# Performance work log

Hardware: AMD Instinct MI355X
Metric: run time of the kernel (lower is better)

The kernel has to match this reference:

```python
import jax, jax.numpy as jnp
import numpy as np

B, N, IN_FEAT, HID, NHEAD, NLAYER, K = 8, 2048, 512, 128, 4, 3, 8
GRAPH_DIM = 32
EPS = 1e-5


def _layernorm(x, g, b):
    m = x.mean(-1, keepdims=True)
    v = ((x - m) ** 2).mean(-1, keepdims=True)
    return (x - m) * jax.lax.rsqrt(v + EPS) * g + b


def _knn_adj(cent):
    # cent [B,Ni,2] -> symmetric bool adjacency [B,Ni,Ni]; each node's k nearest
    # neighbours (self included, dist 0), then bidirected union (to_bidirected).
    d2 = jnp.sum((cent[:, :, None, :] - cent[:, None, :, :]) ** 2, -1)
    _, idx = jax.lax.top_k(-d2, K)  # [B,Ni,K]
    Bc, Nc = cent.shape[0], cent.shape[1]
    mask = jnp.zeros((Bc, Nc, Nc), bool).at[
        jnp.arange(Bc)[:, None, None], jnp.arange(Nc)[None, :, None], idx].set(True)
    return mask | jnp.swapaxes(mask, 1, 2)


def setup_inputs():
    key = jax.random.key(0)
    ks = jax.random.split(key, 12)
    s = 0.05
    H = HID
    return dict(
        feats=jax.random.normal(ks[0], (B, N, IN_FEAT), jnp.float32),
        cent=jax.random.uniform(ks[1], (B, N, 2), jnp.float32),
        Wp1=jax.random.normal(ks[2], (IN_FEAT, H)) * s, bp1=jnp.zeros((H,)),
        bn_g=jnp.ones((H,)), bn_b=jnp.zeros((H,)),
        Wp2=jax.random.normal(ks[3], (H, H)) * s, bp2=jnp.zeros((H,)),
        g1=jnp.ones((NLAYER, H)), be1=jnp.zeros((NLAYER, H)),
        g2=jnp.ones((NLAYER, H)), be2=jnp.zeros((NLAYER, H)),
        Ws=jax.random.normal(ks[4], (NLAYER, NHEAD, H, H)) * s,
        Wn=jax.random.normal(ks[5], (NLAYER, NHEAD, H, H)) * s,
        bs=jnp.zeros((NLAYER, NHEAD, H)),
        Wg=jax.random.normal(ks[6], (NLAYER, NHEAD * H, H)) * s,
        bg=jnp.zeros((NLAYER, H)),
        W1=jax.random.normal(ks[7], (NLAYER, H, H)) * s, b1=jnp.zeros((NLAYER, H)),
        W2=jax.random.normal(ks[8], (NLAYER, H, H)) * s, b2=jnp.zeros((NLAYER, H)),
        Wq=jax.random.normal(ks[9], (NLAYER, H, 1)) * s, bq=jnp.zeros((NLAYER,)),
        Wf1=jax.random.normal(ks[10], (2 * H, H)) * s, bf1=jnp.zeros((H,)),
        Wf2=jax.random.normal(ks[11], (H, GRAPH_DIM)) * s, bf2=jnp.zeros((GRAPH_DIM,)),
    )


def reference(feats, cent, Wp1, bp1, bn_g, bn_b, Wp2, bp2,
              g1, be1, g2, be2, Ws, Wn, bs, Wg, bg,
              W1, b1, W2, b2, Wq, bq, Wf1, bf1, Wf2, bf2):
    # preconv: Linear -> BatchNorm1d(eval: running mean 0 / var 1) -> ReLU -> Linear
    x = feats @ Wp1 + bp1
    x = x * (bn_g / jnp.sqrt(1.0 + EPS)) + bn_b
    x = jax.nn.relu(x) @ Wp2 + bp2              # [B,N,H]
    c = cent
    picks = 0.0
    for i in range(NLAYER):
        A = _knn_adj(c).astype(x.dtype)          # dynamic KNN graph, [B,Ni,Ni]
        deg = A.sum(-1)                          # in-degree (>=1, self loop)
        # GraphTransformerLayer: pre-LN -> multi-head mean SAGEConv -> residual
        xn = _layernorm(x, g1[i], be1[i])
        m = jnp.einsum('bij,bjd->bid', A, xn) / deg[..., None]
        h = jnp.einsum('bnd,hde->bnhe', xn, Ws[i]) \
            + jnp.einsum('bnd,hde->bnhe', m, Wn[i]) + bs[i]
        Bc, Nc = h.shape[0], h.shape[1]
        h = h.reshape(Bc, Nc, NHEAD * HID)       # concat heads on feature dim
        x = x + jax.nn.relu(h) @ Wg[i] + bg[i]
        # FFN block with residual
        xn2 = _layernorm(x, g2[i], be2[i])
        x = x + jax.nn.relu(xn2 @ W1[i] + b1[i]) @ W2[i] + b2[i]
        # SAGPool: GraphConv (symmetric norm) score -> top-k ratio 0.5 -> gate
        dinv = jax.lax.rsqrt(deg)
        s = dinv * jnp.einsum('bij,bj->bi', A, dinv * (x @ Wq[i])[..., 0]) + bq[i]
        kkeep = Nc // 2
        topv, topi = jax.lax.top_k(s, kkeep)     # per-graph top nodes
        x = jnp.take_along_axis(x, topi[..., None], axis=1) * jnp.tanh(topv)[..., None]
        c = jnp.take_along_axis(c, topi[..., None], axis=1)
        # max + avg readout on pooled graph
        picks = picks + jnp.concatenate([x.max(axis=1), x.mean(axis=1)], axis=-1)
    f = jax.nn.relu(picks @ Wf1 + bf1)
    f = jax.nn.relu(f @ Wf2 + bf2)               # [B, GRAPH_DIM]
    return f
```

## Files before the change

### kernel.cpp

```cpp
#include <hip/hip_runtime.h>
#include <math.h>

#define EPSV 1e-5f
#define GF_RELU 1
#define GF_ACCUM 2

typedef unsigned long long u64;
typedef unsigned int u32;
typedef unsigned short u16;
typedef float v2f __attribute__((ext_vector_type(2)));
typedef short bf16x8 __attribute__((ext_vector_type(8)));
typedef float f32x4 __attribute__((ext_vector_type(4)));

static const int Bn = 8;
static const int Nmax = 2048;
static const int KNN_K = 8;

__device__ __forceinline__ u32 split_pack(float v) {
  u32 u = __float_as_uint(v);
  float r = v - __uint_as_float(u & 0xffff0000u);
  return (u >> 16) | (__float_as_uint(r) & 0xffff0000u);
}

__device__ __forceinline__ void split4(float4 v, uint2& hp, uint2& lp) {
  u32 u0 = __float_as_uint(v.x), u1 = __float_as_uint(v.y);
  u32 u2 = __float_as_uint(v.z), u3 = __float_as_uint(v.w);
  float r0 = v.x - __uint_as_float(u0 & 0xffff0000u);
  float r1 = v.y - __uint_as_float(u1 & 0xffff0000u);
  float r2 = v.z - __uint_as_float(u2 & 0xffff0000u);
  float r3 = v.w - __uint_as_float(u3 & 0xffff0000u);
  hp.x = (u0 >> 16) | (u1 & 0xffff0000u);
  hp.y = (u2 >> 16) | (u3 & 0xffff0000u);
  lp.x = (__float_as_uint(r0) >> 16) | (__float_as_uint(r1) & 0xffff0000u);
  lp.y = (__float_as_uint(r2) >> 16) | (__float_as_uint(r3) & 0xffff0000u);
}

__device__ __forceinline__ void depair4(uint4 p, uint2& hp, uint2& lp) {
  hp.x = (p.x & 0xffffu) | (p.y << 16);
  hp.y = (p.z & 0xffffu) | (p.w << 16);
  lp.x = (p.x >> 16) | (p.y & 0xffff0000u);
  lp.y = (p.z >> 16) | (p.w & 0xffff0000u);
}

__global__ void precompute_kernel(const float* __restrict__ bn_g, const float* __restrict__ bn_b,
                                  const float* __restrict__ bp1,
                                  float* __restrict__ sc, float* __restrict__ bb,
                                  float* __restrict__ picks) {
  int t = threadIdx.x;
  if (t < 128) {
    float s = bn_g[t] / sqrtf(1.0f + EPSV);
    sc[t] = s;
    bb[t] = bp1[t] * s + bn_b[t];
  }
  for (int i = t; i < Bn * 256; i += blockDim.x) picks[i] = 0.0f;
}

__global__ void repack_ws_kernel(const float* __restrict__ Ws, const float* __restrict__ Wn,
                                 float* __restrict__ WsP, float* __restrict__ WnP) {
  int idx = blockIdx.x * 256 + threadIdx.x;
  const int total = 3 * 4 * 128 * 128;
  if (idx >= total) return;
  int e = idx & 127, d = (idx >> 7) & 127, h = (idx >> 14) & 3, L = idx >> 16;
  size_t dst = ((size_t)L * 128 + d) * 512 + h * 128 + e;
  WsP[dst] = Ws[idx];
  WnP[dst] = Wn[idx];
}

__global__ void repack_split_kernel(const float* __restrict__ Ws, const float* __restrict__ Wn,
                                    const float* __restrict__ Wg, const float* __restrict__ Wp1,
                                    const float* __restrict__ Wp2, const float* __restrict__ W1,
                                    const float* __restrict__ W2,
                                    u32* __restrict__ Wc,
                                    u16* __restrict__ WgTh, u16* __restrict__ WgTl,
                                    u32* __restrict__ Wp1T, u32* __restrict__ Wp2T,
                                    u16* __restrict__ W1Th, u16* __restrict__ W1Tl,
                                    u16* __restrict__ W2Th, u16* __restrict__ W2Tl) {
  int idx = blockIdx.x * 256 + threadIdx.x;
  if (idx < 393216) {
    int k = idx & 255, col = (idx >> 8) & 511, L = idx >> 17;
    float v;
    if (k < 128)
      v = Ws[(((size_t)(L * 4 + (col >> 7))) * 128 + k) * 128 + (col & 127)];
    else
      v = Wn[(((size_t)(L * 4 + (col >> 7))) * 128 + (k - 128)) * 128 + (col & 127)];
    Wc[idx] = split_pack(v);
  } else if (idx < 589824) {
    int i2 = idx - 393216;
    int k = i2 & 511, col = (i2 >> 9) & 127, L = i2 >> 16;
    u32 pr = split_pack(Wg[((size_t)L * 512 + k) * 128 + col]);
    size_t a = (size_t)L * 65536 + (size_t)(col >> 4) * 8192 +
               (size_t)(k >> 3) * 128 + (col & 15) * 8 + (k & 7);
    WgTh[a] = (u16)pr;
    WgTl[a] = (u16)(pr >> 16);
  } else if (idx < 655360) {
    int i3 = idx - 589824;
    int k = i3 & 511, col = i3 >> 9;
    Wp1T[i3] = split_pack(Wp1[(size_t)k * 128 + col]);
  } else if (idx < 671744) {
    int i4 = idx - 655360;
    int k = i4 & 127, col = i4 >> 7;
    Wp2T[i4] = split_pack(Wp2[(size_t)k * 128 + col]);
  } else if (idx < 720896) {
    int i5 = idx - 671744;
    int k = i5 & 127, col = (i5 >> 7) & 127, L = i5 >> 14;
    u32 pr = split_pack(W1[((size_t)L * 128 + k) * 128 + col]);
    size_t a = (size_t)L * 16384 + (size_t)(col >> 4) * 2048 +
               (size_t)(k >> 3) * 128 + (col & 15) * 8 + (k & 7);
    W1Th[a] = (u16)pr;
    W1Tl[a] = (u16)(pr >> 16);
  } else if (idx < 770048) {
    int i6 = idx - 720896;
    int k = i6 & 127, col = (i6 >> 7) & 127, L = i6 >> 14;
    u32 pr = split_pack(W2[((size_t)L * 128 + k) * 128 + col]);
    size_t a = (size_t)L * 16384 + (size_t)(col >> 4) * 2048 +
               (size_t)(k >> 3) * 128 + (col & 15) * 8 + (k & 7);
    W2Th[a] = (u16)pr;
    W2Tl[a] = (u16)(pr >> 16);
  }
}

template<int T>
__global__ __launch_bounds__(256) void knn_sel_kernel(const float* __restrict__ cent,
                                                      int* __restrict__ knn_idx, int Ni) {
  int i = blockIdx.x * 4 + (threadIdx.x >> 6);
  int b = blockIdx.y, lane = threadIdx.x & 63;
  const float2* cb = (const float2*)(cent + (size_t)b * Ni * 2);
  float2 ci = cb[i];
  u32 d2b[T];
#pragma unroll
  for (int t = 0; t < T; ++t) {
    int j = (t << 6) + lane;
    float2 cj = cb[j];
    float dx = __fsub_rn(ci.x, cj.x);
    float dy = __fsub_rn(ci.y, cj.y);
    float d2 = __fadd_rn(__fmul_rn(dx, dx), __fmul_rn(dy, dy));
    d2b[t] = __float_as_uint(d2);
  }
  constexpr int G = T / 4;
  u32 gmin[G];
  int gidx[G];
#pragma unroll
  for (int g = 0; g < G; ++g) {
    u32 m = d2b[g * 4]; int mi = g * 4;
#pragma unroll
    for (int e = 1; e < 4; ++e) {
      if (d2b[g * 4 + e] < m) { m = d2b[g * 4 + e]; mi = g * 4 + e; }
    }
    gmin[g] = m; gidx[g] = mi;
  }
  for (int r = 0; r < KNN_K; ++r) {
    u32 bd; int bt;
    if (G >= 2) {
      u32 a = gmin[0]; int ai = gidx[0];
      u32 bv = gmin[G / 2]; int bi = gidx[G / 2];
#pragma unroll
      for (int g = 1; g < G / 2; ++g) {
        if (gmin[g] < a) { a = gmin[g]; ai = gidx[g]; }
        if (gmin[G / 2 + g] < bv) { bv = gmin[G / 2 + g]; bi = gidx[G / 2 + g]; }
      }
      bd = a; bt = ai;
      if (bv < bd) { bd = bv; bt = bi; }
    } else {
      bd = gmin[0]; bt = gidx[0];
    }
    u64 key = ((u64)bd << 32) | (u32)((bt << 6) | lane);
    for (int off = 32; off >= 1; off >>= 1) {
      u64 o = __shfl_xor(key, off, 64);
      if (o < key) key = o;
    }
    u32 jsel = (u32)key;
    if (lane == 0) knn_idx[((size_t)(b * Ni + i)) * KNN_K + r] = (int)jsel;
    int tsel = __builtin_amdgcn_readfirstlane((int)(jsel >> 6));
    bool owner = (int)(jsel & 63) == lane;
    int gsel = tsel >> 2;
#pragma unroll
    for (int g = 0; g < G; ++g) {
      if (g == gsel) {
        if (owner) {
#pragma unroll
          for (int e = 0; e < 4; ++e)
            if (g * 4 + e == tsel) d2b[g * 4 + e] = 0xFFFFFFFFu;
          u32 m = d2b[g * 4]; int mi = g * 4;
#pragma unroll
          for (int e = 1; e < 4; ++e)
            if (d2b[g * 4 + e] < m) { m = d2b[g * 4 + e]; mi = g * 4 + e; }
          gmin[g] = m; gidx[g] = mi;
        }
      }
    }
  }
}

__global__ void build_adj_kernel(const int* __restrict__ knn_idx, u32* __restrict__ adj, int Ni) {
  int e = blockIdx.x * blockDim.x + threadIdx.x;
  int total = Bn * Ni * KNN_K;
  if (e >= total) return;
  int b = e / (Ni * KNN_K);
  int rem = e % (Ni * KNN_K);
  int r = rem / KNN_K;
  int j = knn_idx[e];
  atomicOr(&adj[((size_t)(b * Nmax + r)) * 64 + (j >> 5)], 1u << (j & 31));
  atomicOr(&adj[((size_t)(b * Nmax + j)) * 64 + (r >> 5)], 1u << (r & 31));
}

__global__ __launch_bounds__(256) void layernorm_kernel(const float* __restrict__ x,
                                                        const float* __restrict__ g,
                                                        const float* __restrict__ be,
                                                        float* __restrict__ xn) {
  int row = blockIdx.x * 4 + (threadIdx.x >> 6);
  int lane = threadIdx.x & 63;
  const float* xr = x + (size_t)row * 128;
  float v1 = xr[lane], v2 = xr[lane + 64];
  float s = v1 + v2;
  for (int off = 32; off >= 1; off >>= 1) s += __shfl_xor(s, off, 64);
  float mean = s / 128.0f;
  float d1 = v1 - mean, d2 = v2 - mean;
  float q = d1 * d1 + d2 * d2;
  for (int off = 32; off >= 1; off >>= 1) q += __shfl_xor(q, off, 64);
  float rs = rsqrtf(q / 128.0f + EPSV);
  float* xo = xn + (size_t)row * 128;
  xo[lane] = d1 * rs * g[lane] + be[lane];
  xo[lane + 64] = d2 * rs * g[lane + 64] + be[lane + 64];
}

__global__ __launch_bounds__(256) void aggregate_kernel(const u32* __restrict__ adj,
                                                        const float* __restrict__ xn,
                                                        float* __restrict__ m,
                                                        float* __restrict__ dinv, int Ni) {
  int sub = threadIdx.x >> 7;
  int t = threadIdx.x & 127;
  int i = blockIdx.x * 2 + sub, b = blockIdx.y;
  __shared__ int cnt[2];
  extern __shared__ int list[];
  int* lst = list + sub * Ni;
  if (t == 0) cnt[sub] = 0;
  __syncthreads();
  int wpr = Ni >> 5;
  for (int w = t; w < wpr; w += 128) {
    u32 bits = adj[((size_t)(b * Nmax + i)) * 64 + w];
    while (bits) {
      int bit = __ffs(bits) - 1;
      bits &= bits - 1;
      int pos = atomicAdd(&cnt[sub], 1);
      lst[pos] = (w << 5) + bit;
    }
  }
  __syncthreads();
  int d = cnt[sub];
  float a0 = 0.0f, a1 = 0.0f;
  int k = 0;
  for (; k + 2 <= d; k += 2) {
    a0 += xn[((size_t)b * Ni + lst[k]) * 128 + t];
    a1 += xn[((size_t)b * Ni + lst[k + 1]) * 128 + t];
  }
  if (k < d) a0 += xn[((size_t)b * Ni + lst[k]) * 128 + t];
  m[((size_t)b * Ni + i) * 128 + t] = (a0 + a1) / (float)d;
  if (t == 0) dinv[b * Nmax + i] = 1.0f / sqrtf((float)d);
}

__global__ __launch_bounds__(256) void attn_gemm1_kernel(
    const float* __restrict__ XN, const float* __restrict__ MM,
    const u32* __restrict__ Wc, const float* __restrict__ bs,
    u16* __restrict__ Hh, u16* __restrict__ Hl, int M) {
  __shared__ u16 Ah[128][40], Al[128][40], Bh[128][40], Bl[128][40];
  int tid = threadIdx.x;
  int lane = tid & 63, w = tid >> 6;
  int wr = w >> 1, wc = w & 1;
  int lr = lane & 15, lk = (lane >> 4) * 8;
  int rowBase = blockIdx.y * 128, colBase = blockIdx.x * 128;
  f32x4 acc[4][4] = {};
  int arow = tid >> 1, aq = (tid & 1) * 16;
  int bcol = tid >> 1, bq = (tid & 1) * 16;

  float4 af[4];
  uint4 bf[4];
  {
    const float* Ap = XN + (size_t)(rowBase + arow) * 128 + aq;
#pragma unroll
    for (int q = 0; q < 4; ++q) af[q] = *(const float4*)(Ap + 4 * q);
    const u32* Bp = Wc + (size_t)(colBase + bcol) * 256 + bq;
#pragma unroll
    for (int q = 0; q < 4; ++q) bf[q] = *(const uint4*)(Bp + 4 * q);
  }
  for (int t = 0; t < 8; ++t) {
    __syncthreads();
#pragma unroll
    for (int q = 0; q < 4; ++q) {
      uint2 hp, lp;
      split4(af[q], hp, lp);
      *(uint2*)&Ah[arow][aq + 4 * q] = hp;
      *(uint2*)&Al[arow][aq + 4 * q] = lp;
      depair4(bf[q], hp, lp);
      *(uint2*)&Bh[bcol][bq + 4 * q] = hp;
      *(uint2*)&Bl[bcol][bq + 4 * q] = lp;
    }
    __syncthreads();
    if (t + 1 < 8) {
      const float* Asrc = (t + 1 < 4) ? XN : MM;
      int k0 = ((t + 1) & 3) * 32;
      const float* Ap = Asrc + (size_t)(rowBase + arow) * 128 + k0 + aq;
#pragma unroll
      for (int q = 0; q < 4; ++q) af[q] = *(const float4*)(Ap + 4 * q);
      const u32* Bp = Wc + (size_t)(colBase + bcol) * 256 + (t + 1) * 32 + bq;
#pragma unroll
      for (int q = 0; q < 4; ++q) bf[q] = *(const uint4*)(Bp + 4 * q);
    }
    bf16x8 ah[4], al[4], bh[4], bl[4];
#pragma unroll
    for (int mi = 0; mi < 4; ++mi) {
      int ar = wr * 64 + mi * 16 + lr;
      ah[mi] = *(const bf16x8*)&Ah[ar][lk];
      al[mi] = *(const bf16x8*)&Al[ar][lk];
    }
#pragma unroll
    for (int ni = 0; ni < 4; ++ni) {
      int bc = wc * 64 + ni * 16 + lr;
      bh[ni] = *(const bf16x8*)&Bh[bc][lk];
      bl[ni] = *(const bf16x8*)&Bl[bc][lk];
    }
#pragma unroll
    for (int mi = 0; mi < 4; ++mi)
#pragma unroll
      for (int ni = 0; ni < 4; ++ni) {
        f32x4 c = acc[mi][ni];
        c = __builtin_amdgcn_mfma_f32_16x16x32_bf16(al[mi], bh[ni], c, 0, 0, 0);
        c = __builtin_amdgcn_mfma_f32_16x16x32_bf16(ah[mi], bl[ni], c, 0, 0, 0);
        c = __builtin_amdgcn_mfma_f32_16x16x32_bf16(ah[mi], bh[ni], c, 0, 0, 0);
        acc[mi][ni] = c;
      }
  }
  int rq = (lane >> 4) * 4;
#pragma unroll
  for (int ni = 0; ni < 4; ++ni) {
    int col = colBase + wc * 64 + ni * 16 + lr;
    float bv = bs[col];
    size_t cbase = (size_t)(col >> 3) * 128 + (col & 7);
#pragma unroll
    for (int mi = 0; mi < 4; ++mi) {
      int rb = (rowBase >> 4) + wr * 4 + mi;
#pragma unroll
      for (int r = 0; r < 4; ++r) {
        float v = fmaxf(acc[mi][ni][r] + bv, 0.0f);
        u32 pr = split_pack(v);
        size_t o = (size_t)rb * 8192 + cbase + (size_t)(rq + r) * 8;
        Hh[o] = (u16)pr;
        Hl[o] = (u16)(pr >> 16);
      }
    }
  }
}

__global__ __launch_bounds__(256) void attn2_ffn16_kernel(
    const u16* __restrict__ Hh, const u16* __restrict__ Hl,
    const u16* __restrict__ Bgh, const u16* __restrict__ Bgl,
    const float* __restrict__ bg, const float* __restrict__ g,
    const float* __restrict__ be,
    const u16* __restrict__ W1h, const u16* __restrict__ W1l,
    const float* __restrict__ b1,
    const u16* __restrict__ W2h, const u16* __restrict__ W2l,
    const float* __restrict__ b2, float* __restrict__ x,
    const float* __restrict__ Wq, const float* __restrict__ dinv,
    float* __restrict__ PV, int niShift, int M) {
  __shared__ float XF[16][132];
  __shared__ u16 XH[16][136], XL[16][136];
  __shared__ float QS[16];
  int tid = threadIdx.x;
  int lane = tid & 63, w = tid >> 6;
  int lr = lane & 15, lk = (lane >> 4) * 8, rq = (lane >> 4) * 4;
  int rowBase = blockIdx.x * 16;
  int colW = w * 32;
  int fo = (lane >> 4) * 128 + lr * 8;

  f32x4 acc[2] = {};
  {
    const u16* pAh = Hh + (size_t)blockIdx.x * 8192;
    const u16* pAl = Hl + (size_t)blockIdx.x * 8192;
    const u16* pBh = Bgh + (size_t)(w * 2) * 8192;
    const u16* pBl = Bgl + (size_t)(w * 2) * 8192;
    bf16x8 ah = *(const bf16x8*)(pAh + fo);
    bf16x8 al = *(const bf16x8*)(pAl + fo);
    bf16x8 b0h = *(const bf16x8*)(pBh + fo);
    bf16x8 b0l = *(const bf16x8*)(pBl + fo);
    bf16x8 b1h = *(const bf16x8*)(pBh + 8192 + fo);
    bf16x8 b1l = *(const bf16x8*)(pBl + 8192 + fo);
    for (int kt = 0; kt < 16; ++kt) {
      bf16x8 cah = ah, cal = al, cb0h = b0h, cb0l = b0l, cb1h = b1h, cb1l = b1l;
      if (kt + 1 < 16) {
        int off = (kt + 1) * 512 + fo;
        ah = *(const bf16x8*)(pAh + off);
        al = *(const bf16x8*)(pAl + off);
        b0h = *(const bf16x8*)(pBh + off);
        b0l = *(const bf16x8*)(pBl + off);
        b1h = *(const bf16x8*)(pBh + 8192 + off);
        b1l = *(const bf16x8*)(pBl + 8192 + off);
      }
      acc[0] = __builtin_amdgcn_mfma_f32_16x16x32_bf16(cal, cb0h, acc[0], 0, 0, 0);
      acc[0] = __builtin_amdgcn_mfma_f32_16x16x32_bf16(cah, cb0l, acc[0], 0, 0, 0);
      acc[0] = __builtin_amdgcn_mfma_f32_16x16x32_bf16(cah, cb0h, acc[0], 0, 0, 0);
      acc[1] = __builtin_amdgcn_mfma_f32_16x16x32_bf16(cal, cb1h, acc[1], 0, 0, 0);
      acc[1] = __builtin_amdgcn_mfma_f32_16x16x32_bf16(cah, cb1l, acc[1], 0, 0, 0);
      acc[1] = __builtin_amdgcn_mfma_f32_16x16x32_bf16(cah, cb1h, acc[1], 0, 0, 0);
    }
  }
#pragma unroll
  for (int ni = 0; ni < 2; ++ni) {
    int col = colW + ni * 16 + lr;
    float bv = bg[col];
#pragma unroll
    for (int r = 0; r < 4; ++r) {
      int rowL = rq + r;
      size_t o = (size_t)(rowBase + rowL) * 128 + col;
      float v = x[o] + acc[ni][r] + bv;
      x[o] = v;
      XF[rowL][col] = v;
    }
  }
  __syncthreads();
#pragma unroll
  for (int rr = 0; rr < 4; ++rr) {
    int rowL = w * 4 + rr;
    float v1 = XF[rowL][lane], v2 = XF[rowL][64 + lane];
    float s = v1 + v2;
    for (int off = 32; off >= 1; off >>= 1) s += __shfl_xor(s, off, 64);
    float mean = s / 128.0f;
    float d1 = v1 - mean, d2 = v2 - mean;
    float q = d1 * d1 + d2 * d2;
    for (int off = 32; off >= 1; off >>= 1) q += __shfl_xor(q, off, 64);
    float rs = rsqrtf(q / 128.0f + EPSV);
    float xn1 = d1 * rs * g[lane] + be[lane];
    float xn2 = d2 * rs * g[lane + 64] + be[lane + 64];
    u32 p1 = split_pack(xn1);
    u32 p2 = split_pack(xn2);
    XH[rowL][lane] = (u16)p1;  XL[rowL][lane] = (u16)(p1 >> 16);
    XH[rowL][64 + lane] = (u16)p2;  XL[rowL][64 + lane] = (u16)(p2 >> 16);
  }
  __syncthreads();
  f32x4 acc1[2] = {};
  {
    const u16* pBh = W1h + (size_t)(w * 2) * 2048;
    const u16* pBl = W1l + (size_t)(w * 2) * 2048;
#pragma unroll
    for (int kt = 0; kt < 4; ++kt) {
      int k0 = kt * 32 + lk;
      int off = kt * 512 + fo;
      bf16x8 ah = *(const bf16x8*)&XH[lr][k0];
      bf16x8 al = *(const bf16x8*)&XL[lr][k0];
      bf16x8 b0h = *(const bf16x8*)(pBh + off);
      bf16x8 b0l = *(const bf16x8*)(pBl + off);
      bf16x8 b1h = *(const bf16x8*)(pBh + 2048 + off);
      bf16x8 b1l = *(const bf16x8*)(pBl + 2048 + off);
      acc1[0] = __builtin_amdgcn_mfma_f32_16x16x32_bf16(al, b0h, acc1[0], 0, 0, 0);
      acc1[0] = __builtin_amdgcn_mfma_f32_16x16x32_bf16(ah, b0l, acc1[0], 0, 0, 0);
      acc1[0] = __builtin_amdgcn_mfma_f32_16x16x32_bf16(ah, b0h, acc1[0], 0, 0, 0);
      acc1[1] = __builtin_amdgcn_mfma_f32_16x16x32_bf16(al, b1h, acc1[1], 0, 0, 0);
      acc1[1] = __builtin_amdgcn_mfma_f32_16x16x32_bf16(ah, b1l, acc1[1], 0, 0, 0);
      acc1[1] = __builtin_amdgcn_mfma_f32_16x16x32_bf16(ah, b1h, acc1[1], 0, 0, 0);
    }
  }
  __syncthreads();
  if (tid < 16) QS[tid] = 0.0f;
#pragma unroll
  for (int ni = 0; ni < 2; ++ni) {
    int col = colW + ni * 16 + lr;
    float bv = b1[col];
#pragma unroll
    for (int r = 0; r < 4; ++r) {
      int rowL = rq + r;
      float v = fmaxf(acc1[ni][r] + bv, 0.0f);
      u32 pr = split_pack(v);
      XH[rowL][col] = (u16)pr;
      XL[rowL][col] = (u16)(pr >> 16);
    }
  }
  __syncthreads();
  f32x4 acc2[2] = {};
  {
    const u16* pBh = W2h + (size_t)(w * 2) * 2048;
    const u16* pBl = W2l + (size_t)(w * 2) * 2048;
#pragma unroll
    for (int kt = 0; kt < 4; ++kt) {
      int k0 = kt * 32 + lk;
      int off = kt * 512 + fo;
      bf16x8 ah = *(const bf16x8*)&XH[lr][k0];
      bf16x8 al = *(const bf16x8*)&XL[lr][k0];
      bf16x8 b0h = *(const bf16x8*)(pBh + off);
      bf16x8 b0l = *(const bf16x8*)(pBl + off);
      bf16x8 b1h = *(const bf16x8*)(pBh + 2048 + off);
      bf16x8 b1l = *(const bf16x8*)(pBl + 2048 + off);
      acc2[0] = __builtin_amdgcn_mfma_f32_16x16x32_bf16(al, b0h, acc2[0], 0, 0, 0);
      acc2[0] = __builtin_amdgcn_mfma_f32_16x16x32_bf16(ah, b0l, acc2[0], 0, 0, 0);
      acc2[0] = __builtin_amdgcn_mfma_f32_16x16x32_bf16(ah, b0h, acc2[0], 0, 0, 0);
      acc2[1] = __builtin_amdgcn_mfma_f32_16x16x32_bf16(al, b1h, acc2[1], 0, 0, 0);
      acc2[1] = __builtin_amdgcn_mfma_f32_16x16x32_bf16(ah, b1l, acc2[1], 0, 0, 0);
      acc2[1] = __builtin_amdgcn_mfma_f32_16x16x32_bf16(ah, b1h, acc2[1], 0, 0, 0);
    }
  }
  float qp[4] = {0.0f, 0.0f, 0.0f, 0.0f};
#pragma unroll
  for (int ni = 0; ni < 2; ++ni) {
    int col = colW + ni * 16 + lr;
    float bv = b2[col];
    float wq = Wq[col];
#pragma unroll
    for (int r = 0; r < 4; ++r) {
      int rowL = rq + r;
      size_t o = (size_t)(rowBase + rowL) * 128 + col;
      float v = x[o] + acc2[ni][r] + bv;
      x[o] = v;
      qp[r] += v * wq;
    }
  }
#pragma unroll
  for (int r = 0; r < 4; ++r) {
    qp[r] += __shfl_xor(qp[r], 1, 64);
    qp[r] += __shfl_xor(qp[r], 2, 64);
    qp[r] += __shfl_xor(qp[r], 4, 64);
    qp[r] += __shfl_xor(qp[r], 8, 64);
  }
  if (lr == 0) {
#pragma unroll
    for (int r = 0; r < 4; ++r) atomicAdd(&QS[rq + r], qp[r]);
  }
  __syncthreads();
  if (tid < 16) {
    int node = rowBase + tid;
    int bb = node >> niShift;
    int ii = node & ((1 << niShift) - 1);
    PV[bb * Nmax + ii] = dinv[bb * Nmax + ii] * QS[tid];
  }
}

__global__ __launch_bounds__(256) void preconv1_kernel(
    const float* __restrict__ F, const u32* __restrict__ WT,
    const float* __restrict__ sc, const float* __restrict__ bb,
    u32* __restrict__ H, int M) {
  __shared__ u16 Ah[64][40], Al[64][40], Bh[128][40], Bl[128][40];
  int tid = threadIdx.x;
  int lane = tid & 63, w = tid >> 6;
  int wr = w >> 1, wc = w & 1;
  int lr = lane & 15, lk = (lane >> 4) * 8;
  int rowBase = blockIdx.x * 64;
  f32x4 acc[2][4] = {};
  int arow = tid >> 2, aq = (tid & 3) * 8;
  int bcol = tid >> 1, bq = (tid & 1) * 16;

  float4 af[2];
  uint4 bf[4];
  {
    const float* Ap = F + (size_t)(rowBase + arow) * 512 + aq;
    af[0] = *(const float4*)Ap;
    af[1] = *(const float4*)(Ap + 4);
    const u32* Bp = WT + (size_t)bcol * 512 + bq;
#pragma unroll
    for (int q = 0; q < 4; ++q) bf[q] = *(const uint4*)(Bp + 4 * q);
  }
  for (int t = 0; t < 16; ++t) {
    __syncthreads();
    {
      uint2 hp, lp;
      split4(af[0], hp, lp);
      *(uint2*)&Ah[arow][aq] = hp; *(uint2*)&Al[arow][aq] = lp;
      split4(af[1], hp, lp);
      *(uint2*)&Ah[arow][aq + 4] = hp; *(uint2*)&Al[arow][aq + 4] = lp;
#pragma unroll
      for (int q = 0; q < 4; ++q) {
        depair4(bf[q], hp, lp);
        *(uint2*)&Bh[bcol][bq + 4 * q] = hp;
        *(uint2*)&Bl[bcol][bq + 4 * q] = lp;
      }
    }
    __syncthreads();
    if (t + 1 < 16) {
      int k0 = (t + 1) * 32;
      const float* Ap = F + (size_t)(rowBase + arow) * 512 + k0 + aq;
      af[0] = *(const float4*)Ap;
      af[1] = *(const float4*)(Ap + 4);
      const u32* Bp = WT + (size_t)bcol * 512 + k0 + bq;
#pragma unroll
      for (int q = 0; q < 4; ++q) bf[q] = *(const uint4*)(Bp + 4 * q);
    }
    bf16x8 ah[2], al[2], bh[4], bl[4];
#pragma unroll
    for (int mi = 0; mi < 2; ++mi) {
      int ar = wr * 32 + mi * 16 + lr;
      ah[mi] = *(const bf16x8*)&Ah[ar][lk];
      al[mi] = *(const bf16x8*)&Al[ar][lk];
    }
#pragma unroll
    for (int ni = 0; ni < 4; ++ni) {
      int bc = wc * 64 + ni * 16 + lr;
      bh[ni] = *(const bf16x8*)&Bh[bc][lk];
      bl[ni] = *(const bf16x8*)&Bl[bc][lk];
    }
#pragma unroll
    for (int mi = 0; mi < 2; ++mi)
#pragma unroll
      for (int ni = 0; ni < 4; ++ni) {
        f32x4 c = acc[mi][ni];
        c = __builtin_amdgcn_mfma_f32_16x16x32_bf16(al[mi], bh[ni], c, 0, 0, 0);
        c = __builtin_amdgcn_mfma_f32_16x16x32_bf16(ah[mi], bl[ni], c, 0, 0, 0);
        c = __builtin_amdgcn_mfma_f32_16x16x32_bf16(ah[mi], bh[ni], c, 0, 0, 0);
        acc[mi][ni] = c;
      }
  }
  int rq = (lane >> 4) * 4;
#pragma unroll
  for (int ni = 0; ni < 4; ++ni) {
    int col = wc * 64 + ni * 16 + lr;
    float s = sc[col], b = bb[col];
#pragma unroll
    for (int mi = 0; mi < 2; ++mi)
#pragma unroll
      for (int r = 0; r < 4; ++r) {
        int row = rowBase + wr * 32 + mi * 16 + rq + r;
        float v = fmaxf(acc[mi][ni][r] * s + b, 0.0f);
// ... 647 lines not shown
    }
  }
  v2f oacc[4][2] = {};
  {
    float4 q0 = *(const float4*)(W2 + (size_t)bk * 128 + bc);
    float4 q1 = *(const float4*)(W2 + (size_t)bk * 128 + bc + 4);
    for (int kt = 0; kt < 8; ++kt) {
      __syncthreads();
      *(float4*)&Bs[bk * 132 + bc] = q0;
      *(float4*)&Bs[bk * 132 + bc + 4] = q1;
      __syncthreads();
      if (kt < 7) {
        q0 = *(const float4*)(W2 + (size_t)(kt * 16 + 16 + bk) * 128 + bc);
        q1 = *(const float4*)(W2 + (size_t)(kt * 16 + 16 + bk) * 128 + bc + 4);
      }
      int k0 = kt * 16;
#pragma unroll
      for (int kk = 0; kk < 16; ++kk) {
        float av[4];
        v2f bv[2];
        *(float4*)av = *(const float4*)&Hs[(k0 + kk) * 36 + ty * 4];
        *(float4*)&bv[0] = *(const float4*)&Bs[kk * 132 + tx * 4];
#pragma unroll
        for (int r = 0; r < 4; ++r)
#pragma unroll
          for (int c = 0; c < 2; ++c) oacc[r][c] += av[r] * bv[c];
      }
    }
  }
#pragma unroll
  for (int r = 0; r < 4; ++r) {
    int row = rowBase + ty * 4 + r;
    float ov[4];
    *(v2f*)&ov[0] = oacc[r][0];
    *(v2f*)&ov[2] = oacc[r][1];
    float4 old = *(float4*)&x[(size_t)row * 128 + tx * 4];
    float4 v;
    v.x = ov[0] + b2[tx * 4 + 0]; v.x += old.x;
    v.y = ov[1] + b2[tx * 4 + 1]; v.y += old.y;
    v.z = ov[2] + b2[tx * 4 + 2]; v.z += old.z;
    v.w = ov[3] + b2[tx * 4 + 3]; v.w += old.w;
    *(float4*)&x[(size_t)row * 128 + tx * 4] = v;
  }
}

__global__ __launch_bounds__(256) void qp_kernel(const float* __restrict__ x,
                                                 const float* __restrict__ Wq,
                                                 const float* __restrict__ dinv,
                                                 float* __restrict__ p, int Ni) {
  int node = blockIdx.x * 4 + (threadIdx.x >> 6);
  int lane = threadIdx.x & 63;
  int b = node / Ni, i = node % Ni;
  float v = x[(size_t)node * 128 + lane] * Wq[lane] +
            x[(size_t)node * 128 + 64 + lane] * Wq[64 + lane];
  for (int off = 32; off >= 1; off >>= 1) v += __shfl_xor(v, off, 64);
  if (lane == 0) p[b * Nmax + i] = dinv[b * Nmax + i] * v;
}

__global__ __launch_bounds__(256) void score_kernel(const u32* __restrict__ adj,
                                                    const float* __restrict__ p,
                                                    const float* __restrict__ dinv,
                                                    const float* __restrict__ bq,
                                                    float* __restrict__ s, int Ni) {
  int i = blockIdx.x * 4 + (threadIdx.x >> 6);
  int b = blockIdx.y, lane = threadIdx.x & 63;
  int wpr = Ni >> 5;
  float acc = 0.0f;
  if (lane < wpr) {
    u32 bits = adj[((size_t)(b * Nmax + i)) * 64 + lane];
    while (bits) {
      int bit = __ffs(bits) - 1;
      bits &= bits - 1;
      acc += p[b * Nmax + (lane << 5) + bit];
    }
  }
  for (int off = 32; off >= 1; off >>= 1) acc += __shfl_xor(acc, off, 64);
  if (lane == 0) s[b * Nmax + i] = dinv[b * Nmax + i] * acc + bq[0];
}

__global__ void topk_rank_kernel(const float* __restrict__ s, int Ni, int* __restrict__ topi) {
  int b = blockIdx.y;
  int e0 = blockIdx.x * 64;
  int t = threadIdx.x;
  __shared__ u64 keys[2048];
  __shared__ int PR[256];
  for (int e = t; e < Ni; e += 256) {
    u32 u = __float_as_uint(s[b * Nmax + e]);
    u32 mono = (u & 0x80000000u) ? ~u : (u | 0x80000000u);
    keys[e] = ((u64)(~mono) << 32) | (u32)e;
  }
  __syncthreads();
  int quad = t >> 6, eloc = t & 63;
  u64 my = keys[e0 + eloc];
  int seg = Ni >> 2;
  int s0 = quad * seg;
  int rank = 0;
  for (int k = s0; k < s0 + seg; k += 4) {
    rank += (keys[k] < my) ? 1 : 0;
    rank += (keys[k + 1] < my) ? 1 : 0;
    rank += (keys[k + 2] < my) ? 1 : 0;
    rank += (keys[k + 3] < my) ? 1 : 0;
  }
  PR[t] = rank;
  __syncthreads();
  if (t < 64) {
    int tot = PR[t] + PR[t + 64] + PR[t + 128] + PR[t + 192];
    int kkeep = Ni >> 1;
    if (tot < kkeep) topi[b * 1024 + tot] = e0 + t;
  }
}

__global__ __launch_bounds__(256) void gather_pick_kernel(
    const float* __restrict__ x, const float* __restrict__ c,
    const float* __restrict__ s, const int* __restrict__ topi,
    float* __restrict__ xo, float* __restrict__ co,
    const float* __restrict__ g, const float* __restrict__ be,
    float* __restrict__ xn, float* __restrict__ part, int Ni) {
  int gblk = blockIdx.x, b = blockIdx.y;
  int w = threadIdx.x >> 6, lane = threadIdx.x & 63;
  int kkeep = Ni >> 1;
  float mx1 = -INFINITY, mx2 = -INFINITY, sm1 = 0.0f, sm2 = 0.0f;
  for (int r2 = 0; r2 < 8; ++r2) {
    int inew = gblk * 32 + w * 8 + r2;
    int old = topi[b * 1024 + inew];
    float gate = tanhf(s[b * Nmax + old]);
    size_t ri = ((size_t)b * Ni + old) * 128;
    size_t ro = ((size_t)b * kkeep + inew) * 128;
    float v1 = x[ri + lane] * gate;
    float v2 = x[ri + 64 + lane] * gate;
    xo[ro + lane] = v1;
    xo[ro + 64 + lane] = v2;
    if (lane < 2) co[((size_t)b * kkeep + inew) * 2 + lane] = c[((size_t)b * Ni + old) * 2 + lane];
    mx1 = fmaxf(mx1, v1); mx2 = fmaxf(mx2, v2);
    sm1 += v1; sm2 += v2;
    if (g) {
      float sm = v1 + v2;
      for (int off = 32; off >= 1; off >>= 1) sm += __shfl_xor(sm, off, 64);
      float mean = sm / 128.0f;
      float d1 = v1 - mean, d2 = v2 - mean;
      float q = d1 * d1 + d2 * d2;
      for (int off = 32; off >= 1; off >>= 1) q += __shfl_xor(q, off, 64);
      float rs = rsqrtf(q / 128.0f + EPSV);
      xn[ro + lane] = d1 * rs * g[lane] + be[lane];
      xn[ro + 64 + lane] = d2 * rs * g[lane + 64] + be[lane + 64];
    }
  }
  __shared__ float LM[4][128], LS[4][128];
  LM[w][lane] = mx1; LM[w][64 + lane] = mx2;
  LS[w][lane] = sm1; LS[w][64 + lane] = sm2;
  __syncthreads();
  int t = threadIdx.x;
  if (t < 128) {
    float m = fmaxf(fmaxf(LM[0][t], LM[1][t]), fmaxf(LM[2][t], LM[3][t]));
    float ss = (LS[0][t] + LS[1][t]) + (LS[2][t] + LS[3][t]);
    size_t base = ((size_t)(b * (kkeep >> 5) + gblk)) * 256;
    part[base + t] = m;
    part[base + 128 + t] = ss;
  }
}

__global__ void picks_combine_kernel(const float* __restrict__ part, float* __restrict__ picks,
                                     int kkeep, int G) {
  int b = blockIdx.x, t = threadIdx.x;
  float mx = -INFINITY, sm = 0.0f;
  for (int g = 0; g < G; ++g) {
    mx = fmaxf(mx, part[((size_t)(b * G + g)) * 256 + t]);
    sm += part[((size_t)(b * G + g)) * 256 + 128 + t];
  }
  picks[b * 256 + t] += mx;
  picks[b * 256 + 128 + t] += sm / (float)kkeep;
}

__global__ void final_kernel(const float* __restrict__ picks, const float* __restrict__ Wf1,
                             const float* __restrict__ bf1, const float* __restrict__ Wf2,
                             const float* __restrict__ bf2, float* __restrict__ out) {
  int b = blockIdx.x, t = threadIdx.x;
  __shared__ float pk[256];
  __shared__ float fm[128];
  pk[t] = picks[b * 256 + t];
  pk[t + 128] = picks[b * 256 + 128 + t];
  __syncthreads();
  float acc = bf1[t];
  for (int k = 0; k < 256; ++k) acc += pk[k] * Wf1[k * 128 + t];
  fm[t] = fmaxf(acc, 0.0f);
  __syncthreads();
  if (t < 32) {
    float a2 = bf2[t];
    for (int k = 0; k < 128; ++k) a2 += fm[k] * Wf2[k * 32 + t];
    out[b * 32 + t] = fmaxf(a2, 0.0f);
  }
}

extern "C" void kernel_launch(void* const* d_in, const int* in_sizes, int n_in,
                              void* d_out, int out_size, void* d_ws, size_t ws_size,
                              hipStream_t stream) {
  const float* feats = (const float*)d_in[0];
  const float* cent  = (const float*)d_in[1];
  const float* Wp1 = (const float*)d_in[2];
  const float* bp1 = (const float*)d_in[3];
  const float* bn_g = (const float*)d_in[4];
  const float* bn_b = (const float*)d_in[5];
  const float* Wp2 = (const float*)d_in[6];
  const float* bp2 = (const float*)d_in[7];
  const float* g1  = (const float*)d_in[8];
  const float* be1 = (const float*)d_in[9];
  const float* g2  = (const float*)d_in[10];
  const float* be2 = (const float*)d_in[11];
  const float* Ws  = (const float*)d_in[12];
  const float* Wn  = (const float*)d_in[13];
  const float* bs  = (const float*)d_in[14];
  const float* Wg  = (const float*)d_in[15];
  const float* bg  = (const float*)d_in[16];
  const float* W1  = (const float*)d_in[17];
  const float* b1  = (const float*)d_in[18];
  const float* W2  = (const float*)d_in[19];
  const float* b2  = (const float*)d_in[20];
  const float* Wq  = (const float*)d_in[21];
  const float* bq  = (const float*)d_in[22];
  const float* Wf1 = (const float*)d_in[23];
  const float* bf1 = (const float*)d_in[24];
  const float* Wf2 = (const float*)d_in[25];
  const float* bf2 = (const float*)d_in[26];
  float* out = (float*)d_out;

  float* p = (float*)d_ws;
  const size_t SZX = (size_t)Bn * Nmax * 128;
  float* SC = p;    p += 128;
  float* BBv = p;   p += 128;
  float* DINV = p;  p += Bn * Nmax;
  float* PV = p;    p += Bn * Nmax;
  float* SS = p;    p += Bn * Nmax;
  float* PICKS = p; p += Bn * 256;
  float* PART = p;  p += (size_t)Bn * 32 * 256;
  float* C0 = p;    p += (size_t)Bn * Nmax * 2;
  float* C1 = p;    p += (size_t)Bn * Nmax * 2;
  int* KNN = (int*)p;  p += (size_t)Bn * Nmax * KNN_K;
  int* TOPI = (int*)p; p += Bn * 1024;
  u32* ADJ = (u32*)p;  p += (size_t)Bn * Nmax * 64;
  float* X0 = p;    p += SZX;
  float* X1 = p;    p += SZX;
  float* BA = p;    p += SZX;
  float* BB = p;    p += SZX;
  float* HB = p;
  size_t base_floats = (size_t)(p - (float*)d_ws);
  const size_t WPSZ = (size_t)3 * 128 * 512;
  bool fused = ws_size >= (base_floats + 4 * SZX + 2 * WPSZ) * sizeof(float);
  float* WSP = HB + 4 * SZX;
  float* WNP = WSP + WPSZ;
  float* PK = WNP + WPSZ;
  bool fused2 = ws_size >= (base_floats + 8 * SZX + 2 * WPSZ) * sizeof(float);
  bool fused3 = ws_size >= (base_floats + 9 * SZX + 2 * WPSZ) * sizeof(float);

  u16* WgTh = (u16*)PK;
  u16* WgTl = WgTh + 196608;
  u32* Wp1Tu = (u32*)PK + 196608;
  u32* Wp2Tu = Wp1Tu + 65536;
  u32* W1Tu  = Wp2Tu + 16384;
  u16* W1Th = (u16*)W1Tu;
  u16* W1Tl = W1Th + 49152;
  u32* W2Tu  = W1Tu + 49152;
  u16* W2Th = (u16*)W2Tu;
  u16* W2Tl = W2Th + 49152;
  u16* Hh = (u16*)HB;
  u16* Hl = Hh + (size_t)Bn * Nmax * 512;

  hipLaunchKernelGGL(precompute_kernel, dim3(1), dim3(256), 0, stream,
                     bn_g, bn_b, bp1, SC, BBv, PICKS);
  if (fused3) {
    hipLaunchKernelGGL(repack_split_kernel, dim3(3008), dim3(256), 0, stream,
                       Ws, Wn, Wg, Wp1, Wp2, W1, W2,
                       (u32*)WSP, WgTh, WgTl, Wp1Tu, Wp2Tu, W1Th, W1Tl, W2Th, W2Tl);
  } else if (fused) {
    hipLaunchKernelGGL(repack_ws_kernel, dim3(768), dim3(256), 0, stream, Ws, Wn, WSP, WNP);
  }

  const int M0 = Bn * Nmax;
  if (fused3) {
    hipLaunchKernelGGL(preconv1_kernel, dim3(M0 / 64), dim3(256), 0, stream,
                       feats, Wp1Tu, SC, BBv, (u32*)HB, M0);
    hipLaunchKernelGGL(preconv2_ln_kernel, dim3(M0 / 64), dim3(256), 0, stream,
                       (const u32*)HB, Wp2Tu, bp2, g1, be1, X0, BA, M0);
  } else if (fused) {
    hipLaunchKernelGGL(gemm128ks_kernel, dim3(1, M0 / 128, 4), dim3(256), 0, stream,
                       feats, Wp1, HB, M0, 512);
    hipLaunchKernelGGL(gemm_psum4_kernel, dim3(1, M0 / 32), dim3(256), 0, stream,
                       HB, SC, BBv, Wp2, bp2, X0, M0);
  } else {
    hipLaunchKernelGGL(gemm_kernel<32>, dim3(1, M0 / 32), dim3(256), 0, stream,
                       feats, Wp1, (const float*)nullptr, (const float*)nullptr,
                       SC, BBv, BA, M0, 128, 512, GF_RELU);
    hipLaunchKernelGGL(gemm_kernel<32>, dim3(1, M0 / 32), dim3(256), 0, stream,
                       BA, Wp2, (const float*)nullptr, (const float*)nullptr,
                       (const float*)nullptr, bp2, X0, M0, 128, 128, 0);
  }

  float* xc = X0;
  float* xo = X1;
  const float* cc = cent;
  float* co = C0;
  int Ni = Nmax;
  for (int L = 0; L < 3; ++L) {
    int M = Bn * Ni;
    int niShift = (Ni == 2048) ? 11 : (Ni == 1024) ? 10 : 9;
    if (Ni == 2048)      hipLaunchKernelGGL(knn_sel_kernel<32>, dim3(Ni / 4, Bn), dim3(256), 0, stream, cc, KNN, Ni);
    else if (Ni == 1024) hipLaunchKernelGGL(knn_sel_kernel<16>, dim3(Ni / 4, Bn), dim3(256), 0, stream, cc, KNN, Ni);
    else                 hipLaunchKernelGGL(knn_sel_kernel<8>,  dim3(Ni / 4, Bn), dim3(256), 0, stream, cc, KNN, Ni);
    hipMemsetAsync(ADJ, 0, (size_t)Bn * Nmax * 64 * sizeof(u32), stream);
    int tot = Bn * Ni * KNN_K;
    hipLaunchKernelGGL(build_adj_kernel, dim3((tot + 255) / 256), dim3(256), 0, stream,
                       KNN, ADJ, Ni);
    if (!fused3) {
      hipLaunchKernelGGL(layernorm_kernel, dim3(M / 4), dim3(256), 0, stream,
                         xc, g1 + L * 128, be1 + L * 128, BA);
    }
    hipLaunchKernelGGL(aggregate_kernel, dim3(Ni / 2, Bn), dim3(256), 2 * Ni * sizeof(int), stream,
                       ADJ, BA, BB, DINV, Ni);
    if (fused3) {
      hipLaunchKernelGGL(attn_gemm1_kernel, dim3(4, M / 128), dim3(256), 0, stream,
                         BA, BB, (const u32*)WSP + (size_t)L * 512 * 256,
                         bs + L * 512, Hh, Hl, M);
      hipLaunchKernelGGL(attn2_ffn16_kernel, dim3(M / 16), dim3(256), 0, stream,
                         Hh, Hl,
                         WgTh + (size_t)L * 65536, WgTl + (size_t)L * 65536,
                         bg + L * 128, g2 + L * 128, be2 + L * 128,
                         W1Th + (size_t)L * 16384, W1Tl + (size_t)L * 16384,
                         b1 + L * 128,
                         W2Th + (size_t)L * 16384, W2Tl + (size_t)L * 16384,
                         b2 + L * 128, xc,
                         Wq + L * 128, DINV, PV, niShift, M);
    } else if (fused2) {
      hipLaunchKernelGGL(gemm128dual_kernel, dim3(4, M / 128, 2), dim3(256), 0, stream,
                         BA, WSP + (size_t)L * 128 * 512,
                         BB, WNP + (size_t)L * 128 * 512,
                         HB, PK, M, 512);
      hipLaunchKernelGGL(gemm_hsum_kernel, dim3(1, M / 32), dim3(256), 0, stream,
                         HB, PK, bs + L * 512, Wg + (size_t)L * 512 * 128,
                         bg + L * 128, xc, M);
      hipLaunchKernelGGL(layernorm_kernel, dim3(M / 4), dim3(256), 0, stream,
                         xc, g2 + L * 128, be2 + L * 128, BA);
      hipLaunchKernelGGL(ffn_fused_kernel, dim3(M / 32), dim3(256), 0, stream,
                         BA, W1 + (size_t)L * 128 * 128, b1 + L * 128,
                         W2 + (size_t)L * 128 * 128, b2 + L * 128, xc);
    } else if (fused) {
      hipLaunchKernelGGL(gemm128_kernel, dim3(4, M / 128), dim3(256), 0, stream,
                         BA, WSP + (size_t)L * 128 * 512,
                         BB, WNP + (size_t)L * 128 * 512,
                         bs + L * 512, HB, M, 512, 128, GF_RELU);
      hipLaunchKernelGGL(gemm_kernel<32>, dim3(1, M / 32), dim3(256), 0, stream,
                         HB, Wg + (size_t)L * 512 * 128,
                         (const float*)nullptr, (const float*)nullptr,
                         (const float*)nullptr, bg + L * 128,
                         xc, M, 128, 512, GF_ACCUM);
      hipLaunchKernelGGL(layernorm_kernel, dim3(M / 4), dim3(256), 0, stream,
                         xc, g2 + L * 128, be2 + L * 128, BA);
      hipLaunchKernelGGL(ffn_fused_kernel, dim3(M / 32), dim3(256), 0, stream,
                         BA, W1 + (size_t)L * 128 * 128, b1 + L * 128,
                         W2 + (size_t)L * 128 * 128, b2 + L * 128, xc);
    } else {
      for (int hh = 0; hh < 4; ++hh) {
        hipLaunchKernelGGL(gemm_kernel<32>, dim3(1, M / 32), dim3(256), 0, stream,
                           BA, Ws + ((size_t)(L * 4 + hh)) * 128 * 128,
                           BB, Wn + ((size_t)(L * 4 + hh)) * 128 * 128,
                           (const float*)nullptr, bs + (L * 4 + hh) * 128,
                           HB, M, 128, 128, GF_RELU);
        hipLaunchKernelGGL(gemm_kernel<32>, dim3(1, M / 32), dim3(256), 0, stream,
                           HB, Wg + ((size_t)L * 512 + hh * 128) * 128,
                           (const float*)nullptr, (const float*)nullptr,
                           (const float*)nullptr, (hh == 0) ? (bg + L * 128) : (const float*)nullptr,
                           xc, M, 128, 128, GF_ACCUM);
      }
      hipLaunchKernelGGL(layernorm_kernel, dim3(M / 4), dim3(256), 0, stream,
                         xc, g2 + L * 128, be2 + L * 128, BA);
      hipLaunchKernelGGL(ffn_fused_kernel, dim3(M / 32), dim3(256), 0, stream,
                         BA, W1 + (size_t)L * 128 * 128, b1 + L * 128,
                         W2 + (size_t)L * 128 * 128, b2 + L * 128, xc);
    }
    if (!fused3) {
      hipLaunchKernelGGL(qp_kernel, dim3(M / 4), dim3(256), 0, stream, xc, Wq + L * 128, DINV, PV, Ni);
    }
    hipLaunchKernelGGL(score_kernel, dim3(Ni / 4, Bn), dim3(256), 0, stream, ADJ, PV, DINV, bq + L, SS, Ni);
    hipLaunchKernelGGL(topk_rank_kernel, dim3(Ni / 64, Bn), dim3(256), 0, stream,
                       SS, Ni, TOPI);
    int kkeep = Ni >> 1;
    const float* gn = (fused3 && L < 2) ? (g1 + (L + 1) * 128) : (const float*)nullptr;
    const float* bn = (fused3 && L < 2) ? (be1 + (L + 1) * 128) : (const float*)nullptr;
    hipLaunchKernelGGL(gather_pick_kernel, dim3(kkeep / 32, Bn), dim3(256), 0, stream,
                       xc, cc, SS, TOPI, xo, co, gn, bn, BA, PART, Ni);
    int G = kkeep / 32;
    hipLaunchKernelGGL(picks_combine_kernel, dim3(Bn), dim3(128), 0, stream,
                       PART, PICKS, kkeep, G);
    float* tmp = xc; xc = xo; xo = tmp;
    cc = co;
    co = (co == C0) ? C1 : C0;
    Ni = kkeep;
  }
  hipLaunchKernelGGL(final_kernel, dim3(Bn), dim3(128), 0, stream,
                     PICKS, Wf1, bf1, Wf2, bf2, out);
}
```

Before: 494.9 us.

## Fuse kNN adjacency build into selection and pre-split mean features for GEMM

The kNN selection kernel now sets adjacency bits directly with atomics, which removes the separate build_adj kernel and the knn_idx round trip. The memset is moved before the selection launch so the bits start cleared. The aggregate kernel writes the neighbour mean in a pre-split hi/lo bf16 pair layout that matches the MFMA fragments. The first attention GEMM then loads those fragments straight into registers for the second half of K, skipping the LDS staging and split step. The cost is atomics issued inside the selection loop and a more complex load path in the GEMM.

Result: faster. 479.6 us (-3.1%).

```diff
diff --git a/kernel.cpp b/kernel.cpp
--- a/kernel.cpp
+++ b/kernel.cpp
@@ -121,7 +121,7 @@
 
 template<int T>
 __global__ __launch_bounds__(256) void knn_sel_kernel(const float* __restrict__ cent,
-                                                      int* __restrict__ knn_idx, int Ni) {
+                                                      u32* __restrict__ adj, int Ni) {
   int i = blockIdx.x * 4 + (threadIdx.x >> 6);
   int b = blockIdx.y, lane = threadIdx.x & 63;
   const float2* cb = (const float2*)(cent + (size_t)b * Ni * 2);
@@ -169,7 +169,10 @@
       if (o < key) key = o;
     }
     u32 jsel = (u32)key;
-    if (lane == 0) knn_idx[((size_t)(b * Ni + i)) * KNN_K + r] = (int)jsel;
+    if (lane == 0) {
+      atomicOr(&adj[((size_t)(b * Nmax + i)) * 64 + (jsel >> 5)], 1u << (jsel & 31));
+      atomicOr(&adj[((size_t)(b * Nmax + (int)jsel)) * 64 + (i >> 5)], 1u << (i & 31));
+    }
     int tsel = __builtin_amdgcn_readfirstlane((int)(jsel >> 6));
     bool owner = (int)(jsel & 63) == lane;
     int gsel = tsel >> 2;
@@ -189,18 +192,6 @@
       }
     }
   }
-}
-
-__global__ void build_adj_kernel(const int* __restrict__ knn_idx, u32* __restrict__ adj, int Ni) {
-  int e = blockIdx.x * blockDim.x + threadIdx.x;
-  int total = Bn * Ni * KNN_K;
-  if (e >= total) return;
-  int b = e / (Ni * KNN_K);
-  int rem = e % (Ni * KNN_K);
-  int r = rem / KNN_K;
-  int j = knn_idx[e];
-  atomicOr(&adj[((size_t)(b * Nmax + r)) * 64 + (j >> 5)], 1u << (j & 31));
-  atomicOr(&adj[((size_t)(b * Nmax + j)) * 64 + (r >> 5)], 1u << (r & 31));
 }
 
 __global__ __launch_bounds__(256) void layernorm_kernel(const float* __restrict__ x,
@@ -226,6 +217,7 @@
 __global__ __launch_bounds__(256) void aggregate_kernel(const u32* __restrict__ adj,
                                                         const float* __restrict__ xn,
                                                         float* __restrict__ m,
+                                                        u32* __restrict__ mpair,
                                                         float* __restrict__ dinv, int Ni) {
   int sub = threadIdx.x >> 7;
   int t = threadIdx.x & 127;
@@ -254,12 +246,19 @@
     a1 += xn[((size_t)b * Ni + lst[k + 1]) * 128 + t];
   }
   if (k < d) a0 += xn[((size_t)b * Ni + lst[k]) * 128 + t];
-  m[((size_t)b * Ni + i) * 128 + t] = (a0 + a1) / (float)d;
+  float mv = (a0 + a1) / (float)d;
+  if (mpair) {
+    int grow = b * Ni + i;
+    mpair[(size_t)(grow >> 4) * 2048 + (size_t)(t >> 3) * 128 + (grow & 15) * 8 + (t & 7)] =
+        split_pack(mv);
+  } else {
+    m[((size_t)b * Ni + i) * 128 + t] = mv;
+  }
   if (t == 0) dinv[b * Nmax + i] = 1.0f / sqrtf((float)d);
 }
 
 __global__ __launch_bounds__(256) void attn_gemm1_kernel(
-    const float* __restrict__ XN, const float* __restrict__ MM,
+    const float* __restrict__ XN, const u32* __restrict__ MP,
     const u32* __restrict__ Wc, const float* __restrict__ bs,
     u16* __restrict__ Hh, u16* __restrict__ Hl, int M) {
   __shared__ u16 Ah[128][40], Al[128][40], Bh[128][40], Bl[128][40];
@@ -274,6 +273,7 @@
 
   float4 af[4];
   uint4 bf[4];
+  uint4 mp[8];
   {
     const float* Ap = XN + (size_t)(rowBase + arow) * 128 + aq;
 #pragma unroll
@@ -284,33 +284,62 @@
   }
   for (int t = 0; t < 8; ++t) {
     __syncthreads();
+    if (t < 4) {
+#pragma unroll
+      for (int q = 0; q < 4; ++q) {
+        uint2 hp, lp;
+        split4(af[q], hp, lp);
+        *(uint2*)&Ah[arow][aq + 4 * q] = hp;
+        *(uint2*)&Al[arow][aq + 4 * q] = lp;
+      }
+    }
 #pragma unroll
     for (int q = 0; q < 4; ++q) {
       uint2 hp, lp;
-      split4(af[q], hp, lp);
-      *(uint2*)&Ah[arow][aq + 4 * q] = hp;
-      *(uint2*)&Al[arow][aq + 4 * q] = lp;
       depair4(bf[q], hp, lp);
       *(uint2*)&Bh[bcol][bq + 4 * q] = hp;
       *(uint2*)&Bl[bcol][bq + 4 * q] = lp;
     }
     __syncthreads();
+    bf16x8 ah[4], al[4], bh[4], bl[4];
+    if (t < 4) {
+#pragma unroll
+      for (int mi = 0; mi < 4; ++mi) {
+        int ar = wr * 64 + mi * 16 + lr;
+        ah[mi] = *(const bf16x8*)&Ah[ar][lk];
+        al[mi] = *(const bf16x8*)&Al[ar][lk];
+      }
+    } else {
+#pragma unroll
+      for (int mi = 0; mi < 4; ++mi) {
+        uint2 h0, l0, h1, l1;
+        depair4(mp[mi * 2], h0, l0);
+        depair4(mp[mi * 2 + 1], h1, l1);
+        uint4 hx, lx;
+        hx.x = h0.x; hx.y = h0.y; hx.z = h1.x; hx.w = h1.y;
+        lx.x = l0.x; lx.y = l0.y; lx.z = l1.x; lx.w = l1.y;
+        ah[mi] = *(const bf16x8*)&hx;
+        al[mi] = *(const bf16x8*)&lx;
+      }
+    }
+    if (t + 1 < 4) {
+      const float* Ap = XN + (size_t)(rowBase + arow) * 128 + (t + 1) * 32 + aq;
+#pragma unroll
+      for (int q = 0; q < 4; ++q) af[q] = *(const float4*)(Ap + 4 * q);
+    } else if (t + 1 < 8) {
+      int ks = (t + 1 - 4) * 4 + (lane >> 4);
+#pragma unroll
+      for (int mi = 0; mi < 4; ++mi) {
+        const u32* p = MP + (size_t)((rowBase >> 4) + wr * 4 + mi) * 2048 +
+                       (size_t)ks * 128 + lr * 8;
+        mp[mi * 2] = *(const uint4*)p;
+        mp[mi * 2 + 1] = *(const uint4*)(p + 4);
+      }
+    }
     if (t + 1 < 8) {
-      const float* Asrc = (t + 1 < 4) ? XN : MM;
-      int k0 = ((t + 1) & 3) * 32;
-      const float* Ap = Asrc + (size_t)(rowBase + arow) * 128 + k0 + aq;
-#pragma unroll
-      for (int q = 0; q < 4; ++q) af[q] = *(const float4*)(Ap + 4 * q);
       const u32* Bp = Wc + (size_t)(colBase + bcol) * 256 + (t + 1) * 32 + bq;
 #pragma unroll
       for (int q = 0; q < 4; ++q) bf[q] = *(const uint4*)(Bp + 4 * q);
-    }
-    bf16x8 ah[4], al[4], bh[4], bl[4];
-#pragma unroll
-    for (int mi = 0; mi < 4; ++mi) {
-      int ar = wr * 64 + mi * 16 + lr;
-      ah[mi] = *(const bf16x8*)&Ah[ar][lk];
-      al[mi] = *(const bf16x8*)&Al[ar][lk];
     }
 #pragma unroll
     for (int ni = 0; ni < 4; ++ni) {
@@ -1564,22 +1593,20 @@
   for (int L = 0; L < 3; ++L) {
     int M = Bn * Ni;
     int niShift = (Ni == 2048) ? 11 : (Ni == 1024) ? 10 : 9;
-    if (Ni == 2048)      hipLaunchKernelGGL(knn_sel_kernel<32>, dim3(Ni / 4, Bn), dim3(256), 0, stream, cc, KNN, Ni);
-    else if (Ni == 1024) hipLaunchKernelGGL(knn_sel_kernel<16>, dim3(Ni / 4, Bn), dim3(256), 0, stream, cc, KNN, Ni);
-    else                 hipLaunchKernelGGL(knn_sel_kernel<8>,  dim3(Ni / 4, Bn), dim3(256), 0, stream, cc, KNN, Ni);
     hipMemsetAsync(ADJ, 0, (size_t)Bn * Nmax * 64 * sizeof(u32), stream);
-    int tot = Bn * Ni * KNN_K;
-    hipLaunchKernelGGL(build_adj_kernel, dim3((tot + 255) / 256), dim3(256), 0, stream,
-                       KNN, ADJ, Ni);
+    if (Ni == 2048)      hipLaunchKernelGGL(knn_sel_kernel<32>, dim3(Ni / 4, Bn), dim3(256), 0, stream, cc, ADJ, Ni);
+    else if (Ni == 1024) hipLaunchKernelGGL(knn_sel_kernel<16>, dim3(Ni / 4, Bn), dim3(256), 0, stream, cc, ADJ, Ni);
+    else                 hipLaunchKernelGGL(knn_sel_kernel<8>,  dim3(Ni / 4, Bn), dim3(256), 0, stream, cc, ADJ, Ni);
     if (!fused3) {
       hipLaunchKernelGGL(layernorm_kernel, dim3(M / 4), dim3(256), 0, stream,
                          xc, g1 + L * 128, be1 + L * 128, BA);
     }
     hipLaunchKernelGGL(aggregate_kernel, dim3(Ni / 2, Bn), dim3(256), 2 * Ni * sizeof(int), stream,
-                       ADJ, BA, BB, DINV, Ni);
+                       ADJ, BA, fused3 ? (float*)nullptr : BB,
+                       fused3 ? (u32*)BB : (u32*)nullptr, DINV, Ni);
     if (fused3) {
       hipLaunchKernelGGL(attn_gemm1_kernel, dim3(4, M / 128), dim3(256), 0, stream,
-                         BA, BB, (const u32*)WSP + (size_t)L * 512 * 256,
+                         BA, (const u32*)BB, (const u32*)WSP + (size_t)L * 512 * 256,
                          bs + L * 512, Hh, Hl, M);
       hipLaunchKernelGGL(attn2_ffn16_kernel, dim3(M / 16), dim3(256), 0, stream,
                          Hh, Hl,
```
